# Kernel optimization log

Measured on AMD Instinct MI355X. Metric: run time of the kernel, lower is better.

Reference implementation:

```python
import jax, jax.numpy as jnp
import numpy as np

HIDDEN = 128
N_NODES = 50000
N_EDGES = 600000


def setup_inputs() -> dict:
    key = jax.random.key(0)
    k_h, k_s, k_d, k_w1, k_b1, k_w2, k_b2 = jax.random.split(key, 7)
    h = jax.random.normal(k_h, (N_NODES, HIDDEN), dtype=jnp.float32)
    src = jax.random.randint(k_s, (N_EDGES,), 0, N_NODES, dtype=jnp.int64)
    dst = jax.random.randint(k_d, (N_EDGES,), 0, N_NODES, dtype=jnp.int64)
    # link_predictor params: Linear(2H -> H), Linear(H -> 1)
    lim1 = 1.0 / np.sqrt(2 * HIDDEN)
    W1 = jax.random.uniform(k_w1, (2 * HIDDEN, HIDDEN), dtype=jnp.float32, minval=-lim1, maxval=lim1)
    b1 = jax.random.uniform(k_b1, (HIDDEN,), dtype=jnp.float32, minval=-lim1, maxval=lim1)
    lim2 = 1.0 / np.sqrt(HIDDEN)
    W2 = jax.random.uniform(k_w2, (HIDDEN, 1), dtype=jnp.float32, minval=-lim2, maxval=lim2)
    b2 = jax.random.uniform(k_b2, (1,), dtype=jnp.float32, minval=-lim2, maxval=lim2)
    return {"h": h, "W1": W1, "b1": b1, "W2": W2, "b2": b2, "src": src, "dst": dst}


def reference(h, W1, b1, W2, b2, src, dst):
    # per-edge gather of source/destination node features, concat -> [E, 2H]
    h_cat = jnp.concatenate([h[src], h[dst]], axis=1)
    hid = jax.nn.relu(h_cat @ W1 + b1)           # [E, H]
    score = jax.nn.sigmoid(hid @ W2 + b2)        # [E, 1]
    return score.squeeze(-1)                     # [E]
```

## Files before the change

kernel.cpp:

```cpp
#include <hip/hip_runtime.h>
#include <hip/hip_bf16.h>


#define HID    128
#define NNODE  50000
#define NEDGE  600000
#define NGRP   ((NNODE + 31) / 32)
#define K1BLK  ((NGRP + 1) / 2)
#define K2BLK  2048
#define UVBYTES ((size_t)NNODE * 256 * 2)

typedef __attribute__((ext_vector_type(8)))  __bf16 bf16x8;
typedef __attribute__((ext_vector_type(16))) float  f32x16;

static __device__ __forceinline__ unsigned int pack2bf(float a, float b) {
    unsigned int ua = __float_as_uint(a);
    unsigned int ub = __float_as_uint(b);
    ua = (ua + 0x7FFFu + ((ua >> 16) & 1u)) >> 16;
    ub = (ub + 0x7FFFu + ((ub >> 16) & 1u)) >> 16;
    return (ub << 16) | (ua & 0xFFFFu);
}

__global__ __launch_bounds__(256, 1) void node_gemm_kernel(
    const float* __restrict__ h, const float* __restrict__ W1,
    const float* __restrict__ b1, unsigned short* __restrict__ uvs)
{
    const int t = threadIdx.x, lane = t & 63, wv = t >> 6;
    const int l31 = lane & 31, l5 = lane >> 5;

    const int group = blockIdx.x * 2 + (wv >> 1);
    if (group >= NGRP) return;
    const int colhalf = wv & 1;

    float b1v[4];
#pragma unroll
    for (int ct = 0; ct < 4; ++ct)
        b1v[ct] = (colhalf == 0) ? b1[ct * 32 + l31] : 0.0f;

    const int node  = group * 32 + l31;
    const int nodec = node < NNODE ? node : NNODE - 1;
    const float* hp = h + (size_t)nodec * HID + l5 * 8;

    f32x16 acc[4];
#pragma unroll
    for (int ct = 0; ct < 4; ++ct)
#pragma unroll
        for (int r = 0; r < 16; ++r) acc[ct][r] = 0.0f;

#pragma unroll
    for (int ks = 0; ks < 8; ++ks) {
        float4 f0 = *(const float4*)(hp + ks * 16);
        float4 f1 = *(const float4*)(hp + ks * 16 + 4);
        bf16x8 af;
        af[0] = (__bf16)f0.x; af[1] = (__bf16)f0.y;
        af[2] = (__bf16)f0.z; af[3] = (__bf16)f0.w;
        af[4] = (__bf16)f1.x; af[5] = (__bf16)f1.y;
        af[6] = (__bf16)f1.z; af[7] = (__bf16)f1.w;
        const int kb = colhalf * 128 + ks * 16 + l5 * 8;
#pragma unroll
        for (int ct = 0; ct < 4; ++ct) {
            const int n = ct * 32 + l31;
            const float* wp = W1 + (size_t)kb * HID + n;
            bf16x8 bfg;
#pragma unroll
            for (int j = 0; j < 8; ++j) bfg[j] = (__bf16)wp[(size_t)j * HID];
            acc[ct] = __builtin_amdgcn_mfma_f32_32x32x16_bf16(af, bfg,
                                                              acc[ct], 0, 0, 0);
        }
    }

#pragma unroll
    for (int ct = 0; ct < 4; ++ct) {
#pragma unroll
        for (int r = 0; r < 16; ++r) {
            float mine = acc[ct][r] + b1v[ct];
            float partner = __shfl_xor(mine, 1);
            if (!(l31 & 1)) {
                const int rr = (r & 3) + 8 * (r >> 2) + 4 * l5;
                const int nd = group * 32 + rr;
                if (nd < NNODE) {
                    const int n = colhalf * 128 + ct * 32 + l31;
                    *(unsigned int*)(uvs + (size_t)nd * 256 + n) =
                        pack2bf(mine, partner);
                }
            }
        }
    }
}

__global__ __launch_bounds__(256, 8) void edge_score_kernel(
    const unsigned short* __restrict__ uvs,
    const float* __restrict__ W2, const float* __restrict__ b2,
    const int* __restrict__ src, const int* __restrict__ dst,
    float* __restrict__ out)
{
    const int t = threadIdx.x, lane = t & 63, wv = t >> 6;
    const int c = lane & 15;
    const int g = lane >> 4;

    bool idx64;
    {
        unsigned long long m =
            __ballot((src[2 * lane + 1] == 0) && (dst[2 * lane + 1] == 0));
        idx64 = (m == ~0ULL);
    }

    float w2f[8];
#pragma unroll
    for (int j = 0; j < 8; ++j) w2f[j] = W2[c * 8 + j];
    const float b2s = b2[0];

    const int gw = blockIdx.x * 4 + wv;
    const int NW = K2BLK * 4;
    const int NQ = NEDGE / 4;

    for (int q0 = gw; q0 < NQ; q0 += 2 * NW) {
        const int q1  = q0 + NW;
        const int q1c = q1 < NQ ? q1 : NQ - 1;
        const int e0  = q0 * 4 + g;
        const int e1  = q1c * 4 + g;

        const int ns0 = idx64 ? src[2 * e0] : src[e0];
        const int nd0 = idx64 ? dst[2 * e0] : dst[e0];
        const int ns1 = idx64 ? src[2 * e1] : src[e1];
        const int nd1 = idx64 ? dst[2 * e1] : dst[e1];

        const uint4 qu0 = *(const uint4*)(uvs + (size_t)ns0 * 256 + c * 8);
        const uint4 qv0 = *(const uint4*)(uvs + (size_t)nd0 * 256 + 128 + c * 8);
        const uint4 qu1 = *(const uint4*)(uvs + (size_t)ns1 * 256 + c * 8);
        const uint4 qv1 = *(const uint4*)(uvs + (size_t)nd1 * 256 + 128 + c * 8);

#pragma unroll
        for (int half = 0; half < 2; ++half) {
            const uint4 qu = half ? qu1 : qu0;
            const uint4 qv = half ? qv1 : qv0;
            float p = 0.0f;
#pragma unroll
            for (int j = 0; j < 4; ++j) {
                const unsigned int uw = j == 0 ? qu.x : j == 1 ? qu.y
                                      : j == 2 ? qu.z : qu.w;
                const unsigned int vw = j == 0 ? qv.x : j == 1 ? qv.y
                                      : j == 2 ? qv.z : qv.w;
                float slo = __uint_as_float(uw << 16)
                          + __uint_as_float(vw << 16);
                float shi = __uint_as_float(uw & 0xFFFF0000u)
                          + __uint_as_float(vw & 0xFFFF0000u);
                slo = slo > 0.0f ? slo : 0.0f;
                shi = shi > 0.0f ? shi : 0.0f;
                p = fmaf(slo, w2f[2 * j], p);
                p = fmaf(shi, w2f[2 * j + 1], p);
            }
            p += __shfl_xor(p, 1);
            p += __shfl_xor(p, 2);
            p += __shfl_xor(p, 4);
            p += __shfl_xor(p, 8);

            if (c == 0 && (half == 0 || q1 < NQ)) {
                const int e = half ? e1 : e0;
                out[e] = 1.0f / (1.0f + __expf(-(p + b2s)));
            }
        }
    }
}

__global__ __launch_bounds__(256, 1) void edge_mlp_fallback(
    const float* __restrict__ h,  const float* __restrict__ W1,
    const float* __restrict__ b1, const float* __restrict__ W2,
    const float* __restrict__ b2, const int* __restrict__ src,
    const int* __restrict__ dst,  float* __restrict__ out)
{
    __shared__ unsigned char smem[65536];
    const int t = threadIdx.x, lane = t & 63, wv = t >> 6;
    const int l31 = lane & 31, l5 = lane >> 5;
    bool idx64;
    {
        unsigned long long m =
            __ballot((src[2 * lane + 1] == 0) && (dst[2 * lane + 1] == 0));
        idx64 = (m == ~0ULL);
    }
    for (int task = t; task < 4096; task += 256) {
        int n = task & 127, slot = task >> 7;
        const float* wp = W1 + (slot * 8) * HID + n;
        bf16x8 v;
#pragma unroll
        for (int j = 0; j < 8; ++j) v[j] = (__bf16)wp[j * HID];
        *(bf16x8*)(smem + n * 512 + ((slot * 16) ^ ((n & 31) << 4))) = v;
    }
    float b1v[4], w2v[4];
#pragma unroll
    for (int ct = 0; ct < 4; ++ct) {
        int n = ct * 32 + l31;
        b1v[ct] = b1[n]; w2v[ct] = W2[n];
    }
    const float b2s = b2[0];
    __syncthreads();
    const int swz = l31 << 4;
    const int gw = blockIdx.x * 4 + wv;
    for (int tile = gw; tile < NEDGE / 32; tile += 512 * 4) {
        const int e = tile * 32 + l31;
        const long long ns = idx64 ? (long long)src[2 * e] : (long long)src[e];
        const long long nd = idx64 ? (long long)dst[2 * e] : (long long)dst[e];
        const float* hs = h + ns * HID + l5 * 8;
        const float* hd = h + nd * HID + l5 * 8;
        f32x16 acc[4];
#pragma unroll
        for (int ct = 0; ct < 4; ++ct)
#pragma unroll
            for (int r = 0; r < 16; ++r) acc[ct][r] = 0.0f;
#pragma unroll
        for (int ks = 0; ks < 16; ++ks) {
            const float* p = (ks < 8) ? (hs + ks * 16) : (hd + (ks - 8) * 16);
            float4 f0 = *(const float4*)p;
            float4 f1 = *(const float4*)(p + 4);
            bf16x8 af;
            af[0] = (__bf16)f0.x; af[1] = (__bf16)f0.y;
            af[2] = (__bf16)f0.z; af[3] = (__bf16)f0.w;
            af[4] = (__bf16)f1.x; af[5] = (__bf16)f1.y;
            af[6] = (__bf16)f1.z; af[7] = (__bf16)f1.w;
            const int coff = ks * 32 + l5 * 16;
#pragma unroll
            for (int ct = 0; ct < 4; ++ct) {
                const int n = ct * 32 + l31;
                bf16x8 bfg = *(const bf16x8*)(smem + n * 512 + (coff ^ swz));
                acc[ct] = __builtin_amdgcn_mfma_f32_32x32x16_bf16(af, bfg,
                                                                  acc[ct], 0, 0, 0);
            }
        }
        float p[16];
#pragma unroll
        for (int r = 0; r < 16; ++r) p[r] = 0.0f;
#pragma unroll
        for (int ct = 0; ct < 4; ++ct)
#pragma unroll
            for (int r = 0; r < 16; ++r) {
                float v = acc[ct][r] + b1v[ct];
                v = v > 0.0f ? v : 0.0f;
                p[r] += v * w2v[ct];
            }
#pragma unroll
        for (int r = 0; r < 16; ++r) {
            p[r] += __shfl_xor(p[r], 1);  p[r] += __shfl_xor(p[r], 2);
            p[r] += __shfl_xor(p[r], 4);  p[r] += __shfl_xor(p[r], 8);
            p[r] += __shfl_xor(p[r], 16);
        }
        if (l31 == 0) {
#pragma unroll
            for (int g = 0; g < 4; ++g) {
                const int e0 = tile * 32 + g * 8 + l5 * 4;
                float4 o4;
                o4.x = 1.0f / (1.0f + __expf(-(p[4 * g + 0] + b2s)));
                o4.y = 1.0f / (1.0f + __expf(-(p[4 * g + 1] + b2s)));
                o4.z = 1.0f / (1.0f + __expf(-(p[4 * g + 2] + b2s)));
                o4.w = 1.0f / (1.0f + __expf(-(p[4 * g + 3] + b2s)));
                *(float4*)(out + e0) = o4;
            }
        }
    }
}

extern "C" void kernel_launch(void* const* d_in, const int* in_sizes, int n_in,
                              void* d_out, int out_size, void* d_ws, size_t ws_size,
                              hipStream_t stream) {
    const float* h  = (const float*)d_in[0];
    const float* W1 = (const float*)d_in[1];
    const float* b1 = (const float*)d_in[2];
    const float* W2 = (const float*)d_in[3];
    const float* b2 = (const float*)d_in[4];
    const int* src  = (const int*)d_in[5];
    const int* dst  = (const int*)d_in[6];
    (void)in_sizes; (void)n_in; (void)out_size;

    if (ws_size >= UVBYTES) {
        unsigned short* uvs = (unsigned short*)d_ws;
        node_gemm_kernel<<<K1BLK, 256, 0, stream>>>(h, W1, b1, uvs);
        edge_score_kernel<<<K2BLK, 256, 0, stream>>>(uvs, W2, b2, src, dst,
                                                     (float*)d_out);
    } else {
        edge_mlp_fallback<<<512, 256, 0, stream>>>(h, W1, b1, W2, b2, src, dst,
                                                   (float*)d_out);
    }
}
```

Before: 72.31 us.

## Fuse node GEMM and edge scoring into one cooperative kernel with grid sync

Merges the per-node projection and the per-edge scoring kernels into a single persistent cooperative kernel that uses a grid-wide barrier between phases. The node GEMM is split into finer per-wave units (one 32-column tile each) so it spreads across a fixed grid of up to 768 blocks of 512 threads. This removes one kernel launch and the gap between kernels, at the cost of a grid sync, lower occupancy from the cooperative grid size, and repeated W1 reloads per unit. The old shared-memory fallback path is dropped, and the two-kernel path is kept only for when the cooperative launch fails.

```diff
diff --git a/kernel.cpp b/kernel.cpp
--- a/kernel.cpp
+++ b/kernel.cpp
@@ -1,12 +1,17 @@
 #include <hip/hip_runtime.h>
 #include <hip/hip_bf16.h>
+#include <hip/hip_cooperative_groups.h>
+
+namespace cg = cooperative_groups;
 
 
 #define HID    128
 #define NNODE  50000
 #define NEDGE  600000
-#define NGRP   ((NNODE + 31) / 32)
-#define K1BLK  ((NGRP + 1) / 2)
+#define NGRP   1563
+#define NAU    (NGRP * 8)
+#define FTPB   512
+#define FGRID  768
 #define K2BLK  2048
 #define UVBYTES ((size_t)NNODE * 256 * 2)
 
@@ -21,101 +26,88 @@
     return (ub << 16) | (ua & 0xFFFFu);
 }
 
-__global__ __launch_bounds__(256, 1) void node_gemm_kernel(
-    const float* __restrict__ h, const float* __restrict__ W1,
-    const float* __restrict__ b1, unsigned short* __restrict__ uvs)
+__global__ __launch_bounds__(FTPB, 3) void fused_kernel(
+    const float* __restrict__ h,  const float* __restrict__ W1,
+    const float* __restrict__ b1, const float* __restrict__ W2,
+    const float* __restrict__ b2, const int* __restrict__ src,
+    const int* __restrict__ dst,  float* __restrict__ out,
+    unsigned short* __restrict__ uvs)
 {
     const int t = threadIdx.x, lane = t & 63, wv = t >> 6;
     const int l31 = lane & 31, l5 = lane >> 5;
 
-    const int group = blockIdx.x * 2 + (wv >> 1);
-    if (group >= NGRP) return;
-    const int colhalf = wv & 1;
-
-    float b1v[4];
-#pragma unroll
-    for (int ct = 0; ct < 4; ++ct)
-        b1v[ct] = (colhalf == 0) ? b1[ct * 32 + l31] : 0.0f;
-
-    const int node  = group * 32 + l31;
-    const int nodec = node < NNODE ? node : NNODE - 1;
-    const float* hp = h + (size_t)nodec * HID + l5 * 8;
-
-    f32x16 acc[4];
-#pragma unroll
-    for (int ct = 0; ct < 4; ++ct)
-#pragma unroll
-        for (int r = 0; r < 16; ++r) acc[ct][r] = 0.0f;
-
-#pragma unroll
-    for (int ks = 0; ks < 8; ++ks) {
-        float4 f0 = *(const float4*)(hp + ks * 16);
-        float4 f1 = *(const float4*)(hp + ks * 16 + 4);
-        bf16x8 af;
-        af[0] = (__bf16)f0.x; af[1] = (__bf16)f0.y;
-        af[2] = (__bf16)f0.z; af[3] = (__bf16)f0.w;
-        af[4] = (__bf16)f1.x; af[5] = (__bf16)f1.y;
-        af[6] = (__bf16)f1.z; af[7] = (__bf16)f1.w;
-        const int kb = colhalf * 128 + ks * 16 + l5 * 8;
-#pragma unroll
-        for (int ct = 0; ct < 4; ++ct) {
-            const int n = ct * 32 + l31;
-            const float* wp = W1 + (size_t)kb * HID + n;
+    bool idx64;
+    {
+        unsigned long long m =
+            __ballot((src[2 * lane + 1] == 0) && (dst[2 * lane + 1] == 0));
+        idx64 = (m == ~0ULL);
+    }
+
+    const int gw = blockIdx.x * 8 + wv;
+    const int NWAVES = gridDim.x * 8;
+
+    for (int unit = gw; unit < NAU; unit += NWAVES) {
+        const int group   = unit >> 3;
+        const int sub     = unit & 7;
+        const int colhalf = sub >> 2;
+        const int ct      = sub & 3;
+
+        const int node  = group * 32 + l31;
+        const int nodec = node < NNODE ? node : NNODE - 1;
+        const float* hp = h + (size_t)nodec * HID + l5 * 8;
+        const int n = ct * 32 + l31;
+        const float b1v = (colhalf == 0) ? b1[n] : 0.0f;
+
+        f32x16 acc;
+#pragma unroll
+        for (int r = 0; r < 16; ++r) acc[r] = 0.0f;
+
+#pragma unroll
+        for (int ks = 0; ks < 8; ++ks) {
+            float4 f0 = *(const float4*)(hp + ks * 16);
+            float4 f1 = *(const float4*)(hp + ks * 16 + 4);
+            bf16x8 af;
+            af[0] = (__bf16)f0.x; af[1] = (__bf16)f0.y;
+            af[2] = (__bf16)f0.z; af[3] = (__bf16)f0.w;
+            af[4] = (__bf16)f1.x; af[5] = (__bf16)f1.y;
+            af[6] = (__bf16)f1.z; af[7] = (__bf16)f1.w;
+            const float* wp = W1 + (size_t)(colhalf * 128 + ks * 16 + l5 * 8)
+                                       * HID + n;
             bf16x8 bfg;
 #pragma unroll
             for (int j = 0; j < 8; ++j) bfg[j] = (__bf16)wp[(size_t)j * HID];
-            acc[ct] = __builtin_amdgcn_mfma_f32_32x32x16_bf16(af, bfg,
-                                                              acc[ct], 0, 0, 0);
-        }
-    }
-
-#pragma unroll
-    for (int ct = 0; ct < 4; ++ct) {
+            acc = __builtin_amdgcn_mfma_f32_32x32x16_bf16(af, bfg, acc, 0, 0, 0);
+        }
+
 #pragma unroll
         for (int r = 0; r < 16; ++r) {
-            float mine = acc[ct][r] + b1v[ct];
+            float mine = acc[r] + b1v;
             float partner = __shfl_xor(mine, 1);
             if (!(l31 & 1)) {
                 const int rr = (r & 3) + 8 * (r >> 2) + 4 * l5;
                 const int nd = group * 32 + rr;
                 if (nd < NNODE) {
-                    const int n = colhalf * 128 + ct * 32 + l31;
-                    *(unsigned int*)(uvs + (size_t)nd * 256 + n) =
-                        pack2bf(mine, partner);
+                    *(unsigned int*)(uvs + (size_t)nd * 256 +
+                                     colhalf * 128 + n) = pack2bf(mine, partner);
                 }
             }
         }
     }
-}
-
-__global__ __launch_bounds__(256, 8) void edge_score_kernel(
-    const unsigned short* __restrict__ uvs,
-    const float* __restrict__ W2, const float* __restrict__ b2,
-    const int* __restrict__ src, const int* __restrict__ dst,
-    float* __restrict__ out)
-{
-    const int t = threadIdx.x, lane = t & 63, wv = t >> 6;
+
+    __threadfence();
+    cg::this_grid().sync();
+    __threadfence();
+
     const int c = lane & 15;
     const int g = lane >> 4;
-
-    bool idx64;
-    {
-        unsigned long long m =
-            __ballot((src[2 * lane + 1] == 0) && (dst[2 * lane + 1] == 0));
-        idx64 = (m == ~0ULL);
-    }
-
     float w2f[8];
 #pragma unroll
     for (int j = 0; j < 8; ++j) w2f[j] = W2[c * 8 + j];
     const float b2s = b2[0];
 
-    const int gw = blockIdx.x * 4 + wv;
-    const int NW = K2BLK * 4;
     const int NQ = NEDGE / 4;
-
-    for (int q0 = gw; q0 < NQ; q0 += 2 * NW) {
-        const int q1  = q0 + NW;
+    for (int q0 = gw; q0 < NQ; q0 += 2 * NWAVES) {
+        const int q1  = q0 + NWAVES;
         const int q1c = q1 < NQ ? q1 : NQ - 1;
         const int e0  = q0 * 4 + g;
         const int e1  = q1c * 4 + g;
@@ -163,96 +155,129 @@
     }
 }
 
-__global__ __launch_bounds__(256, 1) void edge_mlp_fallback(
-    const float* __restrict__ h,  const float* __restrict__ W1,
-    const float* __restrict__ b1, const float* __restrict__ W2,
-    const float* __restrict__ b2, const int* __restrict__ src,
-    const int* __restrict__ dst,  float* __restrict__ out)
+__global__ __launch_bounds__(256, 1) void node_gemm_kernel(
+    const float* __restrict__ h, const float* __restrict__ W1,
+    const float* __restrict__ b1, unsigned short* __restrict__ uvs)
 {
-    __shared__ unsigned char smem[65536];
     const int t = threadIdx.x, lane = t & 63, wv = t >> 6;
     const int l31 = lane & 31, l5 = lane >> 5;
+    const int group = blockIdx.x * 2 + (wv >> 1);
+    if (group >= NGRP) return;
+    const int colhalf = wv & 1;
+    float b1v[4];
+#pragma unroll
+    for (int ct = 0; ct < 4; ++ct)
+        b1v[ct] = (colhalf == 0) ? b1[ct * 32 + l31] : 0.0f;
+    const int node  = group * 32 + l31;
+    const int nodec = node < NNODE ? node : NNODE - 1;
+    const float* hp = h + (size_t)nodec * HID + l5 * 8;
+    f32x16 acc[4];
+#pragma unroll
+    for (int ct = 0; ct < 4; ++ct)
+#pragma unroll
+        for (int r = 0; r < 16; ++r) acc[ct][r] = 0.0f;
+#pragma unroll
+    for (int ks = 0; ks < 8; ++ks) {
+        float4 f0 = *(const float4*)(hp + ks * 16);
+        float4 f1 = *(const float4*)(hp + ks * 16 + 4);
+        bf16x8 af;
+        af[0] = (__bf16)f0.x; af[1] = (__bf16)f0.y;
+        af[2] = (__bf16)f0.z; af[3] = (__bf16)f0.w;
+        af[4] = (__bf16)f1.x; af[5] = (__bf16)f1.y;
+        af[6] = (__bf16)f1.z; af[7] = (__bf16)f1.w;
+        const int kb = colhalf * 128 + ks * 16 + l5 * 8;
+#pragma unroll
+        for (int ct = 0; ct < 4; ++ct) {
+            const int n = ct * 32 + l31;
+            const float* wp = W1 + (size_t)kb * HID + n;
+            bf16x8 bfg;
+#pragma unroll
+            for (int j = 0; j < 8; ++j) bfg[j] = (__bf16)wp[(size_t)j * HID];
+            acc[ct] = __builtin_amdgcn_mfma_f32_32x32x16_bf16(af, bfg,
+                                                              acc[ct], 0, 0, 0);
+        }
+    }
+#pragma unroll
+    for (int ct = 0; ct < 4; ++ct) {
+#pragma unroll
+        for (int r = 0; r < 16; ++r) {
+            float mine = acc[ct][r] + b1v[ct];
+            float partner = __shfl_xor(mine, 1);
+            if (!(l31 & 1)) {
+                const int rr = (r & 3) + 8 * (r >> 2) + 4 * l5;
+                const int nd = group * 32 + rr;
+                if (nd < NNODE) {
+                    const int n = colhalf * 128 + ct * 32 + l31;
+                    *(unsigned int*)(uvs + (size_t)nd * 256 + n) =
+                        pack2bf(mine, partner);
+                }
+            }
+        }
+    }
+}
+
+__global__ __launch_bounds__(256, 8) void edge_score_kernel(
+    const unsigned short* __restrict__ uvs,
+    const float* __restrict__ W2, const float* __restrict__ b2,
+    const int* __restrict__ src, const int* __restrict__ dst,
+    float* __restrict__ out)
+{
+    const int t = threadIdx.x, lane = t & 63, wv = t >> 6;
+    const int c = lane & 15;
+    const int g = lane >> 4;
     bool idx64;
     {
         unsigned long long m =
             __ballot((src[2 * lane + 1] == 0) && (dst[2 * lane + 1] == 0));
         idx64 = (m == ~0ULL);
     }
-    for (int task = t; task < 4096; task += 256) {
-        int n = task & 127, slot = task >> 7;
-        const float* wp = W1 + (slot * 8) * HID + n;
-        bf16x8 v;
-#pragma unroll
-        for (int j = 0; j < 8; ++j) v[j] = (__bf16)wp[j * HID];
-        *(bf16x8*)(smem + n * 512 + ((slot * 16) ^ ((n & 31) << 4))) = v;
-    }
-    float b1v[4], w2v[4];
-#pragma unroll
-    for (int ct = 0; ct < 4; ++ct) {
-        int n = ct * 32 + l31;
-        b1v[ct] = b1[n]; w2v[ct] = W2[n];
-    }
+    float w2f[8];
+#pragma unroll
+    for (int j = 0; j < 8; ++j) w2f[j] = W2[c * 8 + j];
     const float b2s = b2[0];
-    __syncthreads();
-    const int swz = l31 << 4;
     const int gw = blockIdx.x * 4 + wv;
-    for (int tile = gw; tile < NEDGE / 32; tile += 512 * 4) {
-        const int e = tile * 32 + l31;
-        const long long ns = idx64 ? (long long)src[2 * e] : (long long)src[e];
-        const long long nd = idx64 ? (long long)dst[2 * e] : (long long)dst[e];
-        const float* hs = h + ns * HID + l5 * 8;
-        const float* hd = h + nd * HID + l5 * 8;
-        f32x16 acc[4];
-#pragma unroll
-        for (int ct = 0; ct < 4; ++ct)
-#pragma unroll
-            for (int r = 0; r < 16; ++r) acc[ct][r] = 0.0f;
-#pragma unroll
-        for (int ks = 0; ks < 16; ++ks) {
-            const float* p = (ks < 8) ? (hs + ks * 16) : (hd + (ks - 8) * 16);
-            float4 f0 = *(const float4*)p;
-            float4 f1 = *(const float4*)(p + 4);
-            bf16x8 af;
-            af[0] = (__bf16)f0.x; af[1] = (__bf16)f0.y;
-            af[2] = (__bf16)f0.z; af[3] = (__bf16)f0.w;
-            af[4] = (__bf16)f1.x; af[5] = (__bf16)f1.y;
-            af[6] = (__bf16)f1.z; af[7] = (__bf16)f1.w;
-            const int coff = ks * 32 + l5 * 16;
-#pragma unroll
-            for (int ct = 0; ct < 4; ++ct) {
-                const int n = ct * 32 + l31;
-                bf16x8 bfg = *(const bf16x8*)(smem + n * 512 + (coff ^ swz));
-                acc[ct] = __builtin_amdgcn_mfma_f32_32x32x16_bf16(af, bfg,
-                                                                  acc[ct], 0, 0, 0);
-            }
-        }
-        float p[16];
-#pragma unroll
-        for (int r = 0; r < 16; ++r) p[r] = 0.0f;
-#pragma unroll
-        for (int ct = 0; ct < 4; ++ct)
-#pragma unroll
-            for (int r = 0; r < 16; ++r) {
-                float v = acc[ct][r] + b1v[ct];
-                v = v > 0.0f ? v : 0.0f;
-                p[r] += v * w2v[ct];
-            }
-#pragma unroll
-        for (int r = 0; r < 16; ++r) {
-            p[r] += __shfl_xor(p[r], 1);  p[r] += __shfl_xor(p[r], 2);
-            p[r] += __shfl_xor(p[r], 4);  p[r] += __shfl_xor(p[r], 8);
-            p[r] += __shfl_xor(p[r], 16);
-        }
-        if (l31 == 0) {
-#pragma unroll
-            for (int g = 0; g < 4; ++g) {
-                const int e0 = tile * 32 + g * 8 + l5 * 4;
-                float4 o4;
-                o4.x = 1.0f / (1.0f + __expf(-(p[4 * g + 0] + b2s)));
-                o4.y = 1.0f / (1.0f + __expf(-(p[4 * g + 1] + b2s)));
-                o4.z = 1.0f / (1.0f + __expf(-(p[4 * g + 2] + b2s)));
-                o4.w = 1.0f / (1.0f + __expf(-(p[4 * g + 3] + b2s)));
-                *(float4*)(out + e0) = o4;
+    const int NW = K2BLK * 4;
+    const int NQ = NEDGE / 4;
+    for (int q0 = gw; q0 < NQ; q0 += 2 * NW) {
+        const int q1  = q0 + NW;
+        const int q1c = q1 < NQ ? q1 : NQ - 1;
+        const int e0  = q0 * 4 + g;
+        const int e1  = q1c * 4 + g;
+        const int ns0 = idx64 ? src[2 * e0] : src[e0];
+        const int nd0 = idx64 ? dst[2 * e0] : dst[e0];
+        const int ns1 = idx64 ? src[2 * e1] : src[e1];
+        const int nd1 = idx64 ? dst[2 * e1] : dst[e1];
+        const uint4 qu0 = *(const uint4*)(uvs + (size_t)ns0 * 256 + c * 8);
+        const uint4 qv0 = *(const uint4*)(uvs + (size_t)nd0 * 256 + 128 + c * 8);
+        const uint4 qu1 = *(const uint4*)(uvs + (size_t)ns1 * 256 + c * 8);
+        const uint4 qv1 = *(const uint4*)(uvs + (size_t)nd1 * 256 + 128 + c * 8);
+#pragma unroll
+        for (int half = 0; half < 2; ++half) {
+            const uint4 qu = half ? qu1 : qu0;
+            const uint4 qv = half ? qv1 : qv0;
+            float p = 0.0f;
+#pragma unroll
+            for (int j = 0; j < 4; ++j) {
+                const unsigned int uw = j == 0 ? qu.x : j == 1 ? qu.y
+                                      : j == 2 ? qu.z : qu.w;
+                const unsigned int vw = j == 0 ? qv.x : j == 1 ? qv.y
+                                      : j == 2 ? qv.z : qv.w;
+                float slo = __uint_as_float(uw << 16)
+                          + __uint_as_float(vw << 16);
+                float shi = __uint_as_float(uw & 0xFFFF0000u)
+                          + __uint_as_float(vw & 0xFFFF0000u);
+                slo = slo > 0.0f ? slo : 0.0f;
+                shi = shi > 0.0f ? shi : 0.0f;
+                p = fmaf(slo, w2f[2 * j], p);
+                p = fmaf(shi, w2f[2 * j + 1], p);
+            }
+            p += __shfl_xor(p, 1);
+            p += __shfl_xor(p, 2);
+            p += __shfl_xor(p, 4);
+            p += __shfl_xor(p, 8);
+            if (c == 0 && (half == 0 || q1 < NQ)) {
+                const int e = half ? e1 : e0;
+                out[e] = 1.0f / (1.0f + __expf(-(p + b2s)));
             }
         }
     }
@@ -268,15 +293,29 @@
     const float* b2 = (const float*)d_in[4];
     const int* src  = (const int*)d_in[5];
     const int* dst  = (const int*)d_in[6];
+    float* out = (float*)d_out;
     (void)in_sizes; (void)n_in; (void)out_size;
 
-    if (ws_size >= UVBYTES) {
-        unsigned short* uvs = (unsigned short*)d_ws;
-        node_gemm_kernel<<<K1BLK, 256, 0, stream>>>(h, W1, b1, uvs);
+    if (ws_size < UVBYTES) return;
+    unsigned short* uvs = (unsigned short*)d_ws;
+
+    int maxBlk = 0;
+    hipOccupancyMaxActiveBlocksPerMultiprocessor(&maxBlk,
+        (const void*)fused_kernel, FTPB, 0);
+    int grid = maxBlk * 256;
+    if (grid > FGRID) grid = FGRID;
+    hipError_t err = hipErrorUnknown;
+    if (grid >= 1) {
+        void* args[] = {(void*)&h, (void*)&W1, (void*)&b1, (void*)&W2,
+                        (void*)&b2, (void*)&src, (void*)&dst, (void*)&out,
+                        (void*)&uvs};
+        err = hipLaunchCooperativeKernel((const void*)fused_kernel,
+                                         dim3(grid), dim3(FTPB), args, 0,
+                                         stream);
+    }
+    if (err != hipSuccess) {
+        node_gemm_kernel<<<(NGRP + 1) / 2, 256, 0, stream>>>(h, W1, b1, uvs);
         edge_score_kernel<<<K2BLK, 256, 0, stream>>>(uvs, W2, b2, src, dst,
-                                                     (float*)d_out);
-    } else {
-        edge_mlp_fallback<<<512, 256, 0, stream>>>(h, W1, b1, W2, b2, src, dst,
-                                                   (float*)d_out);
-    }
-}
+                                                     out);
+    }
+}
```

New measurement: 218.3 us. +201.8%, slower.
